# Performance work log

Measured on AMD Instinct MI355X. Metric: run time of the kernel, lower is better.

## Reference

```python
import jax, jax.numpy as jnp
import numpy as np

N, E, F_IN, HID, H, NCLS, L = 100000, 1600000, 128, 128, 4, 40, 2
C = HID // H  # per-head channels = 32
LN_EPS = 1e-5
SOFTMAX_EPS = 1e-16  # PyG softmax denominator epsilon


def setup_inputs() -> dict:
    key = jax.random.key(0)
    ks = jax.random.split(key, 8)
    s = 1.0 / np.sqrt(F_IN).astype(np.float32)
    return {
        "x": jax.random.normal(ks[0], (N, F_IN), jnp.float32),
        "edge_index": jax.random.randint(ks[1], (2, E), 0, N, jnp.int32),
        "Wq": jax.random.normal(ks[2], (L, F_IN, HID), jnp.float32) * s,
        "bq": jnp.zeros((L, HID), jnp.float32),
        "Wk": jax.random.normal(ks[3], (L, F_IN, HID), jnp.float32) * s,
        "bk": jnp.zeros((L, HID), jnp.float32),
        "Wv": jax.random.normal(ks[4], (L, F_IN, HID), jnp.float32) * s,
        "bv": jnp.zeros((L, HID), jnp.float32),
        "Ws": jax.random.normal(ks[5], (L, F_IN, HID), jnp.float32) * s,
        "bs": jnp.zeros((L, HID), jnp.float32),
        "gamma": jnp.ones((L, HID), jnp.float32),
        "beta": jnp.zeros((L, HID), jnp.float32),
        "Wout": jax.random.normal(ks[6], (HID, NCLS), jnp.float32) * (1.0 / np.sqrt(HID).astype(np.float32)),
        "bout": jnp.zeros((NCLS,), jnp.float32),
    }


def _transformer_conv(x, src, dst, Wq, bq, Wk, bk, Wv, bv, Ws, bs):
    # PyG TransformerConv, concat=False, root_weight=True, beta=False
    n = x.shape[0]
    q = (x @ Wq + bq).reshape(n, H, C)
    k = (x @ Wk + bk).reshape(n, H, C)
    v = (x @ Wv + bv).reshape(n, H, C)
    # per-edge attention logits: [E, H]
    alpha = jnp.einsum('ehc,ehc->eh', q[dst], k[src]) / np.sqrt(C).astype(np.float32)
    # segment softmax over incoming edges of each destination node
    amax = jax.ops.segment_max(alpha, dst, num_segments=n)        # [N, H]
    ex = jnp.exp(alpha - amax[dst])                               # [E, H]
    denom = jax.ops.segment_sum(ex, dst, num_segments=n)         # [N, H]
    w = ex / (denom[dst] + SOFTMAX_EPS)                           # [E, H]
    msg = v[src] * w[:, :, None]                                  # [E, H, C]
    out = jax.ops.segment_sum(msg, dst, num_segments=n)          # [N, H, C]
    out = out.mean(axis=1)                                        # concat=False -> head average, [N, C*?]. Here C*H==HID only via mean over H of C dims -> [N, C]
    # NOTE: concat=False averages heads -> [N, C]; skip proj maps in->C? In PyG, out_channels=hidden here,
    # so lin_* are Linear(in, heads*hidden)... but TransformerConv(in, hidden) means out_channels=hidden/?
    return out


def _conv(x, src, dst, Wq, bq, Wk, bk, Wv, bv, Ws, bs):
    # Faithful version with out_channels = HID per head? No: TransformerConv(in, hidden, heads, concat=False)
    # in PyG uses out_channels=hidden and lin_* : in -> heads*out_channels. To keep HID total width we model
    # per-head dim C = HID // H (standard multi-head factorization with same total width HID).
    n = x.shape[0]
    q = (x @ Wq + bq).reshape(n, H, C)
    k = (x @ Wk + bk).reshape(n, H, C)
    v = (x @ Wv + bv).reshape(n, H, C)
    alpha = jnp.einsum('ehc,ehc->eh', q[dst], k[src]) / np.sqrt(C).astype(np.float32)
    amax = jax.ops.segment_max(alpha, dst, num_segments=n)
    ex = jnp.exp(alpha - amax[dst])
    denom = jax.ops.segment_sum(ex, dst, num_segments=n)
    w = ex / (denom[dst] + SOFTMAX_EPS)
    msg = (v[src] * w[:, :, None]).reshape(-1, H * C)             # [E, HID]
    agg = jax.ops.segment_sum(msg, dst, num_segments=n)          # [N, HID]
    # concat=False -> mean over heads, then broadcast back is not what PyG does; PyG yields [N, out_channels].
    out = agg.reshape(n, H, C).mean(axis=1)                       # [N, C]
    out = jnp.tile(out, (1, H))                                   # widen back to HID? No — instead use skip of width HID.
    return out


def _conv_layer(x, src, dst, Wq, bq, Wk, bk, Wv, bv, Ws, bs):
    """TransformerConv(in, HID, heads=H, concat=False): lin_{q,k,v}: in -> H*HID is too wide for a
    memory target, so we use the equivalent standard factorization HID = H*C (per-head C), giving
    attention output [N, H, C]; concat=False head-mean is applied per head group and the result is
    projected residually via lin_skip (in -> HID)."""
    n = x.shape[0]
    q = (x @ Wq + bq).reshape(n, H, C)
    k = (x @ Wk + bk).reshape(n, H, C)
    v = (x @ Wv + bv).reshape(n, H, C)
    alpha = jnp.einsum('ehc,ehc->eh', q[dst], k[src]) / np.sqrt(C).astype(np.float32)
    amax = jax.ops.segment_max(alpha, dst, num_segments=n)        # [N, H]
    ex = jnp.exp(alpha - amax[dst])                               # [E, H]
    denom = jax.ops.segment_sum(ex, dst, num_segments=n)
    w = ex / (denom[dst] + SOFTMAX_EPS)
    msg = (v[src] * w[:, :, None]).reshape(-1, HID)               # [E, HID] (head-concat)
    agg = jax.ops.segment_sum(msg, dst, num_segments=n)          # [N, HID]
    return agg + x @ Ws + bs                                      # root/skip connection


def _layernorm(h, g, b):
    mu = h.mean(-1, keepdims=True)
    var = ((h - mu) ** 2).mean(-1, keepdims=True)
    return (h - mu) * jax.lax.rsqrt(var + LN_EPS) * g + b


def reference(x, edge_index, Wq, bq, Wk, bk, Wv, bv, Ws, bs, gamma, beta, Wout, bout):
    src, dst = edge_index[0], edge_index[1]
    h = x
    for l in range(L):  # fixed small layer count
        h = _conv_layer(h, src, dst, Wq[l], bq[l], Wk[l], bk[l], Wv[l], bv[l], Ws[l], bs[l])
        h = jax.nn.relu(_layernorm(h, gamma[l], beta[l]))
        # dropout is identity in eval mode
    return h @ Wout + bout  # [N, NCLS]
```

## Files before the change

kernel.cpp:

```cpp
#include <hip/hip_runtime.h>
#include <math.h>

#define N_NODES 100000
#define N_EDGES 1600000
#define NCLS_ 40
#define NSCAN_BLOCKS ((N_NODES + 1023) / 1024)
#define DRANGE 12500
#define SRCS_PAD (N_EDGES + 3 * N_NODES + 64)

#define QSCALE (0.17677669529663687f * 1.4426950408889634f)

#if __has_builtin(__builtin_amdgcn_exp2f)
#define EXP2(x) __builtin_amdgcn_exp2f(x)
#else
#define EXP2(x) exp2f(x)
#endif

typedef short bf16x8 __attribute__((ext_vector_type(8)));
typedef float f32x4 __attribute__((ext_vector_type(4)));

__device__ __forceinline__ unsigned short f2b(float f) {
    union { float f; unsigned u; } v; v.f = f;
    unsigned r = v.u + 0x7fffu + ((v.u >> 16) & 1u);
    return (unsigned short)(r >> 16);
}
__device__ __forceinline__ unsigned cvtpk(float x, float y) {
    unsigned r;
    asm("v_cvt_pk_bf16_f32 %0, %1, %2" : "=v"(r) : "v"(x), "v"(y));
    return r;
}
__device__ __forceinline__ float2 up2(unsigned u) {
    union { unsigned u; float f; } a, b;
    a.u = u << 16; b.u = u & 0xffff0000u;
    return make_float2(a.f, b.f);
}
__device__ __forceinline__ float b2f(unsigned short s) {
    union { unsigned u; float f; } v; v.u = ((unsigned)s) << 16;
    return v.f;
}


__global__ void zero_i32_kernel(int* __restrict__ p, int n) {
    int i = blockIdx.x * blockDim.x + threadIdx.x;
    if (i < n) p[i] = 0;
}

__global__ __launch_bounds__(256) void wconv_kernel(
    const float* __restrict__ Wq, const float* __restrict__ Wk,
    const float* __restrict__ Wv, const float* __restrict__ Ws,
    unsigned short* __restrict__ Wbf) {
    int tid = blockIdx.x * 256 + threadIdx.x;
    if (tid >= 131072) return;
    int k   = tid & 127;
    int n   = (tid >> 7) & 63;
    int g   = (tid >> 13) & 1;
    int mat = (tid >> 14) & 3;
    int l   = tid >> 16;
    const float* W = (mat == 0) ? Wq : (mat == 1) ? Wk : (mat == 2) ? Wv : Ws;
    float w = W[l * 16384 + k * 128 + g * 64 + n];
    if (mat == 0) w *= QSCALE;
    Wbf[tid] = f2b(w);
}

__global__ __launch_bounds__(256) void hist_kernel(
    const int* __restrict__ dst, int* __restrict__ deg) {
    int group = blockIdx.x & 7;
    int gblk  = blockIdx.x >> 3;
    int nblk  = gridDim.x >> 3;
    int lo = group * DRANGE, hi = lo + DRANGE;
    for (int i = gblk * 256 + threadIdx.x; i < N_EDGES; i += nblk * 256) {
        int d = dst[i];
        if (d >= lo && d < hi) atomicAdd(&deg[d], 1);
    }
}

__global__ __launch_bounds__(1024) void scan_block_kernel(
    const int* __restrict__ deg, int* __restrict__ rowptr, int* __restrict__ sums) {
    __shared__ int tmp[1024];
    int t = threadIdx.x;
    int i = blockIdx.x * 1024 + t;
    int v = (i < N_NODES) ? ((deg[i] + 3) & ~3) : 0;
    tmp[t] = v;
    __syncthreads();
    for (int d = 1; d < 1024; d <<= 1) {
        int add = (t >= d) ? tmp[t - d] : 0;
        __syncthreads();
        tmp[t] += add;
        __syncthreads();
    }
    if (i < N_NODES) rowptr[i] = tmp[t] - v;
    if (t == 1023) sums[blockIdx.x] = tmp[1023];
}

__global__ __launch_bounds__(128) void scan_sums_kernel(int* __restrict__ sums) {
    __shared__ int tmp[128];
    int t = threadIdx.x;
    int v = (t < NSCAN_BLOCKS) ? sums[t] : 0;
    tmp[t] = v;
    __syncthreads();
    for (int d = 1; d < 128; d <<= 1) {
        int add = (t >= d) ? tmp[t - d] : 0;
        __syncthreads();
        tmp[t] += add;
        __syncthreads();
    }
    if (t < NSCAN_BLOCKS) sums[t] = tmp[t] - v;
}

__global__ void scan_add_kernel(int* __restrict__ rowptr, const int* __restrict__ sums,
                                int* __restrict__ cursor) {
    int i = blockIdx.x * blockDim.x + threadIdx.x;
    if (i < N_NODES) {
        int val = rowptr[i] + sums[i >> 10];
        rowptr[i] = val;
        cursor[i] = val;
    }
}

__global__ __launch_bounds__(256) void scatter_kernel(
    const int* __restrict__ src, const int* __restrict__ dst,
    int* __restrict__ cursor, int* __restrict__ srcs) {
    int group = blockIdx.x & 7;
    int gblk  = blockIdx.x >> 3;
    int nblk  = gridDim.x >> 3;
    int lo = group * DRANGE, hi = lo + DRANGE;
    for (int i = gblk * 256 + threadIdx.x; i < N_EDGES; i += nblk * 256) {
        int d = dst[i];
        if (d >= lo && d < hi) {
            int pos = atomicAdd(&cursor[d], 1);
            srcs[pos] = src[i] << 10;
        }
    }
}

__global__ __launch_bounds__(512, 4) void gemm_qkvs_kernel(
    const void* __restrict__ Ap, int a_is_bf16,
    const unsigned short* __restrict__ Wbf,
    const float* __restrict__ b0, const float* __restrict__ b1,
    const float* __restrict__ b2, const float* __restrict__ b3,
    unsigned short* __restrict__ out) {
    __shared__ unsigned short Bs[2][64][138];
    int t = threadIdx.x;
    int row0 = blockIdx.x * 128;
    int wr = t >> 6, lane = t & 63;
    int ln = lane & 15, quad = lane >> 4;
    int node = row0 + wr * 16 + ln;
    int nodeC = (node < N_NODES) ? node : (N_NODES - 1);

    bf16x8 aF[4];
    if (a_is_bf16) {
        const unsigned short* ar = (const unsigned short*)Ap + (size_t)nodeC * 128;
        #pragma unroll
        for (int ks = 0; ks < 4; ++ks)
            aF[ks] = *(const bf16x8*)&ar[ks * 32 + quad * 8];
    } else {
        const float* ar = (const float*)Ap + (size_t)nodeC * 128;
        #pragma unroll
        for (int ks = 0; ks < 4; ++ks) {
            float4 f0 = *(const float4*)&ar[ks * 32 + quad * 8];
            float4 f1 = *(const float4*)&ar[ks * 32 + quad * 8 + 4];
            union { unsigned u[4]; bf16x8 v; } cv;
            cv.u[0] = cvtpk(f0.x, f0.y);
            cv.u[1] = cvtpk(f0.z, f0.w);
            cv.u[2] = cvtpk(f1.x, f1.y);
            cv.u[3] = cvtpk(f1.z, f1.w);
            aF[ks] = cv.v;
        }
    }

    ushort4 pf[4];
    {
        const unsigned short* Wg = Wbf;
        #pragma unroll
        for (int i = 0; i < 4; ++i) {
            int idx = t + i * 512;
            pf[i] = *(const ushort4*)&Wg[((idx >> 5) << 7) + ((idx & 31) << 2)];
        }
        #pragma unroll
        for (int i = 0; i < 4; ++i) {
            int idx = t + i * 512;
            *(ushort4*)&Bs[0][idx >> 5][(idx & 31) << 2] = pf[i];
        }
    }
    __syncthreads();

    bool ok = node < N_NODES;
    #pragma unroll
    for (int g = 0; g < 8; ++g) {
        int mat = g >> 1;
        int cur = g & 1;
        const float* bias = (mat == 0) ? b0 : (mat == 1) ? b1 : (mat == 2) ? b2 : b3;
        int cb = (g & 1) * 64;

        if (g < 7) {
            const unsigned short* Wg = Wbf + (size_t)(g + 1) * 8192;
            #pragma unroll
            for (int i = 0; i < 4; ++i) {
                int idx = t + i * 512;
                pf[i] = *(const ushort4*)&Wg[((idx >> 5) << 7) + ((idx & 31) << 2)];
            }
        }

        f32x4 acc[4];
        #pragma unroll
        for (int c = 0; c < 4; ++c) acc[c] = (f32x4){0.f, 0.f, 0.f, 0.f};
        #pragma unroll
        for (int ks = 0; ks < 4; ++ks) {
            int k0 = ks * 32 + quad * 8;
            #pragma unroll
            for (int c = 0; c < 4; ++c) {
                bf16x8 w = *(bf16x8*)&Bs[cur][c * 16 + ln][k0];
                acc[c] = __builtin_amdgcn_mfma_f32_16x16x32_bf16(w, aF[ks], acc[c], 0, 0, 0);
            }
        }

        #pragma unroll
        for (int c = 0; c < 4; ++c) {
            int ch = cb + c * 16 + quad * 4;
            float4 bb = *(const float4*)&bias[ch];
            float s = (mat == 0) ? QSCALE : 1.0f;
            float v0 = acc[c][0] + bb.x * s;
            float v1 = acc[c][1] + bb.y * s;
            float v2 = acc[c][2] + bb.z * s;
            float v3 = acc[c][3] + bb.w * s;
            int pos;
            if (mat == 0)      pos = ch;
            else if (mat == 3) pos = 384 + ch;
            else               pos = 128 + (ch << 1) + ((mat == 2) ? 4 : 0);
            if (ok) {
                uint2 wd;
                wd.x = cvtpk(v0, v1);
                wd.y = cvtpk(v2, v3);
                *(uint2*)&out[(size_t)node * 512 + pos] = wd;
            }
        }

        if (g < 7) {
            int nxt = cur ^ 1;
            #pragma unroll
            for (int i = 0; i < 4; ++i) {
                int idx = t + i * 512;
                *(ushort4*)&Bs[nxt][idx >> 5][(idx & 31) << 2] = pf[i];
            }
        }
        __syncthreads();
    }
}

#define EDGE(KV, ECOND) {                                            \
        float2 k01 = up2(KV.x), k23 = up2(KV.y);                     \
        float p = q01.x*k01.x + q01.y*k01.y + q23.x*k23.x + q23.y*k23.y; \
        p += __shfl_xor(p, 1);                                       \
        p += __shfl_xor(p, 2);                                       \
        p += __shfl_xor(p, 4);                                       \
        float e = (ECOND);                                           \
        float2 v01 = up2(KV.z), v23 = up2(KV.w);                     \
        a0 = fmaf(e, v01.x, a0); a1 = fmaf(e, v01.y, a1);            \
        a2 = fmaf(e, v23.x, a2); a3 = fmaf(e, v23.y, a3);            \
        dsum += e; }

__global__ __launch_bounds__(256) void edge_fused_kernel(
    const unsigned short* __restrict__ qkvs,
    const int* __restrict__ srcs, const int* __restrict__ rowptr,
    const int* __restrict__ deg,
    const float* __restrict__ gamma, const float* __restrict__ beta,
    unsigned short* __restrict__ hout) {
    int n = (blockIdx.x * 256 + threadIdx.x) >> 6;
    int lane = threadIdx.x & 63;
    if (n >= N_NODES) return;
    int half = lane >> 5, hl = lane & 31;
    const unsigned short* qrow = qkvs + (size_t)n * 512;
    uint2 qu = *(const uint2*)&qrow[4 * hl];
    float2 q01 = up2(qu.x), q23 = up2(qu.y);
    uint2 su = *(const uint2*)&qrow[384 + 4 * hl];
    float2 sk01 = up2(su.x), sk23 = up2(su.y);
    int e0 = rowptr[n];
    int rem = deg[n];
    const char* kbase = (const char*)qkvs + 256 + 16 * hl;
    const int* sb = srcs + e0 + 4 * half;
    float a0 = 0.f, a1 = 0.f, a2 = 0.f, a3 = 0.f, dsum = 0.f;

    int4 oc;
    if (rem >= 8) oc = *(const int4*)sb;
    while (rem >= 8) {
        int4 on;
        if (rem >= 16) on = *(const int4*)(sb + 8);
        uint4 kv0 = *(const uint4*)(kbase + (unsigned)oc.x);
        uint4 kv1 = *(const uint4*)(kbase + (unsigned)oc.y);
        uint4 kv2 = *(const uint4*)(kbase + (unsigned)oc.z);
        uint4 kv3 = *(const uint4*)(kbase + (unsigned)oc.w);
        EDGE(kv0, EXP2(p));
        EDGE(kv1, EXP2(p));
        EDGE(kv2, EXP2(p));
        EDGE(kv3, EXP2(p));
        oc = on; sb += 8; rem -= 8;
    }
    if (rem > 0) {
        int4 ot = *(const int4*)sb;
        int tb = 4 * half;
        uint4 kv0 = *(const uint4*)(kbase + (unsigned)ot.x);
        uint4 kv1 = *(const uint4*)(kbase + (unsigned)ot.y);
        uint4 kv2 = *(const uint4*)(kbase + (unsigned)ot.z);
        uint4 kv3 = *(const uint4*)(kbase + (unsigned)ot.w);
        EDGE(kv0, (tb + 0 < rem) ? EXP2(p) : 0.f);
        EDGE(kv1, (tb + 1 < rem) ? EXP2(p) : 0.f);
        EDGE(kv2, (tb + 2 < rem) ? EXP2(p) : 0.f);
        EDGE(kv3, (tb + 3 < rem) ? EXP2(p) : 0.f);
    }

    a0 += __shfl_xor(a0, 32); a1 += __shfl_xor(a1, 32);
    a2 += __shfl_xor(a2, 32); a3 += __shfl_xor(a3, 32);
    dsum += __shfl_xor(dsum, 32);
    float dinv = 1.0f / (dsum + 1e-16f);
    float o0 = a0 * dinv + sk01.x, o1 = a1 * dinv + sk01.y;
    float o2 = a2 * dinv + sk23.x, o3 = a3 * dinv + sk23.y;
    float sum = o0 + o1 + o2 + o3;
    for (int m = 1; m < 64; m <<= 1) sum += __shfl_xor(sum, m);
    float mu = sum * (1.0f / 256.0f);
    float d0 = o0 - mu, d1 = o1 - mu, d2 = o2 - mu, d3 = o3 - mu;
    float sq = d0 * d0 + d1 * d1 + d2 * d2 + d3 * d3;
    for (int m = 1; m < 64; m <<= 1) sq += __shfl_xor(sq, m);
    float rs = rsqrtf(sq * (1.0f / 256.0f) + 1e-5f);
    if (half == 0) {
        float4 g4 = *(const float4*)&gamma[4 * hl];
        float4 b4 = *(const float4*)&beta[4 * hl];
        float r0 = fmaxf(d0 * rs * g4.x + b4.x, 0.f);
        float r1 = fmaxf(d1 * rs * g4.y + b4.y, 0.f);
        float r2 = fmaxf(d2 * rs * g4.z + b4.z, 0.f);
        float r3 = fmaxf(d3 * rs * g4.w + b4.w, 0.f);
        uint2 w;
        w.x = cvtpk(r0, r1);
        w.y = cvtpk(r2, r3);
        *(uint2*)&hout[(size_t)n * 128 + 4 * hl] = w;
    }
}

__global__ __launch_bounds__(256) void out_gemm_kernel(
    const unsigned short* __restrict__ h, const float* __restrict__ Wout,
    const float* __restrict__ bout, float* __restrict__ out) {
    int wv = __builtin_amdgcn_readfirstlane((int)(threadIdx.x >> 6));
    int l = threadIdx.x & 63;
    int n = blockIdx.x * 64 + l;
    int jb = wv * 10;
    int nc = (n < N_NODES) ? n : (N_NODES - 1);
    const unsigned short* hrow = h + (size_t)nc * 128;
    uint4 hp[16];
    #pragma unroll
    for (int i = 0; i < 16; ++i) hp[i] = *(const uint4*)&hrow[i * 8];
    float acc[10];
    #pragma unroll
    for (int j = 0; j < 10; ++j) acc[j] = bout[jb + j];
    #pragma unroll
    for (int i = 0; i < 16; ++i) {
        float2 c01 = up2(hp[i].x), c23 = up2(hp[i].y);
        float2 c45 = up2(hp[i].z), c67 = up2(hp[i].w);
        float hc0 = c01.x, hc1 = c01.y, hc2 = c23.x, hc3 = c23.y;
        float hc4 = c45.x, hc5 = c45.y, hc6 = c67.x, hc7 = c67.y;
        #pragma unroll
        for (int j = 0; j < 10; ++j) {
            const float* wk = Wout + (i * 8) * NCLS_ + jb + j;
            acc[j] = fmaf(hc0, wk[0 * NCLS_], acc[j]);
            acc[j] = fmaf(hc1, wk[1 * NCLS_], acc[j]);
            acc[j] = fmaf(hc2, wk[2 * NCLS_], acc[j]);
            acc[j] = fmaf(hc3, wk[3 * NCLS_], acc[j]);
            acc[j] = fmaf(hc4, wk[4 * NCLS_], acc[j]);
            acc[j] = fmaf(hc5, wk[5 * NCLS_], acc[j]);
            acc[j] = fmaf(hc6, wk[6 * NCLS_], acc[j]);
            acc[j] = fmaf(hc7, wk[7 * NCLS_], acc[j]);
        }
    }
    if (n < N_NODES) {
        #pragma unroll
        for (int j = 0; j < 10; ++j) out[(size_t)n * NCLS_ + jb + j] = acc[j];
    }
}

extern "C" void kernel_launch(void* const* d_in, const int* in_sizes, int n_in,
                              void* d_out, int out_size, void* d_ws, size_t ws_size,
                              hipStream_t stream) {
    const float* x    = (const float*)d_in[0];
    const int*   ei   = (const int*)d_in[1];
    const int*   src  = ei;
    const int*   dst  = ei + N_EDGES;
    const float* Wq   = (const float*)d_in[2];
    const float* bq   = (const float*)d_in[3];
    const float* Wk   = (const float*)d_in[4];
    const float* bk   = (const float*)d_in[5];
    const float* Wv   = (const float*)d_in[6];
    const float* bv   = (const float*)d_in[7];
    const float* Wsk  = (const float*)d_in[8];
    const float* bsk  = (const float*)d_in[9];
    const float* gmm  = (const float*)d_in[10];
    const float* bta  = (const float*)d_in[11];
    const float* Wout = (const float*)d_in[12];
    const float* bout = (const float*)d_in[13];
    float* outp = (float*)d_out;

    char* p = (char*)d_ws;
    auto carve = [&](size_t bytes) {
        char* r = p;
        p += (bytes + 255) & ~(size_t)255;
        return r;
    };
    unsigned short* qkvs = (unsigned short*)carve((size_t)N_NODES * 512 * 2);
    unsigned short* h    = (unsigned short*)carve((size_t)N_NODES * 128 * 2);
    unsigned short* Wbf  = (unsigned short*)carve((size_t)131072 * 2);
    int* deg     = (int*)carve((size_t)N_NODES * 4);
    int* rowptr  = (int*)carve((size_t)(N_NODES + 1) * 4);
    int* cursor  = (int*)carve((size_t)N_NODES * 4);
    int* srcs    = (int*)carve((size_t)SRCS_PAD * 4);
    int* sums    = (int*)carve((size_t)NSCAN_BLOCKS * 4);

    wconv_kernel<<<512, 256, 0, stream>>>(Wq, Wk, Wv, Wsk, Wbf);

    zero_i32_kernel<<<(N_NODES + 255) / 256, 256, 0, stream>>>(deg, N_NODES);
    zero_i32_kernel<<<(SRCS_PAD + 255) / 256, 256, 0, stream>>>(srcs, SRCS_PAD);
    hist_kernel<<<2048, 256, 0, stream>>>(dst, deg);
    scan_block_kernel<<<NSCAN_BLOCKS, 1024, 0, stream>>>(deg, rowptr, sums);
    scan_sums_kernel<<<1, 128, 0, stream>>>(sums);
    scan_add_kernel<<<(N_NODES + 255) / 256, 256, 0, stream>>>(rowptr, sums, cursor);
    scatter_kernel<<<2048, 256, 0, stream>>>(src, dst, cursor, srcs);

    for (int l = 0; l < 2; ++l) {
        const void* hin = l ? (const void*)h : (const void*)x;
        gemm_qkvs_kernel<<<(N_NODES + 127) / 128, 512, 0, stream>>>(
            hin, l, Wbf + (size_t)l * 65536,
            bq + l * 128, bk + l * 128, bv + l * 128, bsk + l * 128, qkvs);
        edge_fused_kernel<<<(N_NODES + 3) / 4, 256, 0, stream>>>(
            qkvs, srcs, rowptr, deg, gmm + l * 128, bta + l * 128, h);
    }
    out_gemm_kernel<<<(N_NODES + 63) / 64, 256, 0, stream>>>(h, Wout, bout, outp);
}
```

Before: 681.5 us.

## Pre-swizzle weights into MFMA fragment order and fold srcs padding zeroing into scan

The weight conversion kernel now writes bf16 weights already in per-lane MFMA fragment order. The GEMM can then copy each weight tile to LDS with contiguous 16-byte loads and read fragments without a padded, strided layout. The output columns are permuted so each lane writes wider contiguous stores. The separate full zeroing of the padded srcs array is removed, and scan_add now zeroes only each node's padding slots plus a tail. This relies on the deg/rowptr padding convention matching the rest of the code.

New measurement: 671.8 us. Within noise of the previous version (-1.4%).

```diff
diff --git a/kernel.cpp b/kernel.cpp
--- a/kernel.cpp
+++ b/kernel.cpp
@@ -51,13 +51,18 @@
     unsigned short* __restrict__ Wbf) {
     int tid = blockIdx.x * 256 + threadIdx.x;
     if (tid >= 131072) return;
-    int k   = tid & 127;
-    int n   = (tid >> 7) & 63;
-    int g   = (tid >> 13) & 1;
-    int mat = (tid >> 14) & 3;
-    int l   = tid >> 16;
+    int j     = tid & 7;
+    int lane  = (tid >> 3) & 63;
+    int ks    = (tid >> 9) & 3;
+    int c     = (tid >> 11) & 3;
+    int ghalf = (tid >> 13) & 1;
+    int mat   = (tid >> 14) & 3;
+    int l     = tid >> 16;
+    int ln = lane & 15, quad = lane >> 4;
+    int col = ghalf * 64 + ((ln >> 2) << 4) + (c << 2) + (ln & 3);
+    int krow = (ks << 5) + (quad << 3) + j;
     const float* W = (mat == 0) ? Wq : (mat == 1) ? Wk : (mat == 2) ? Wv : Ws;
-    float w = W[l * 16384 + k * 128 + g * 64 + n];
+    float w = W[l * 16384 + krow * 128 + col];
     if (mat == 0) w *= QSCALE;
     Wbf[tid] = f2b(w);
 }
@@ -108,12 +113,20 @@
 }
 
 __global__ void scan_add_kernel(int* __restrict__ rowptr, const int* __restrict__ sums,
-                                int* __restrict__ cursor) {
+                                const int* __restrict__ deg,
+                                int* __restrict__ cursor, int* __restrict__ srcs) {
     int i = blockIdx.x * blockDim.x + threadIdx.x;
     if (i < N_NODES) {
         int val = rowptr[i] + sums[i >> 10];
         rowptr[i] = val;
         cursor[i] = val;
+        int d = deg[i];
+        int pad = ((d + 3) & ~3);
+        for (int j = d; j < pad; ++j) srcs[val + j] = 0;
+        if (i == N_NODES - 1) {
+            int end = val + pad;
+            for (int j = 0; j < 16; ++j) srcs[end + j] = 0;
+        }
     }
 }
 
@@ -139,7 +152,7 @@
     const float* __restrict__ b0, const float* __restrict__ b1,
     const float* __restrict__ b2, const float* __restrict__ b3,
     unsigned short* __restrict__ out) {
-    __shared__ unsigned short Bs[2][64][138];
+    __shared__ unsigned short WL[2][8192];
     int t = threadIdx.x;
     int row0 = blockIdx.x * 128;
     int wr = t >> 6, lane = t & 63;
@@ -168,19 +181,11 @@
         }
     }
 
-    ushort4 pf[4];
     {
-        const unsigned short* Wg = Wbf;
-        #pragma unroll
-        for (int i = 0; i < 4; ++i) {
-            int idx = t + i * 512;
-            pf[i] = *(const ushort4*)&Wg[((idx >> 5) << 7) + ((idx & 31) << 2)];
-        }
-        #pragma unroll
-        for (int i = 0; i < 4; ++i) {
-            int idx = t + i * 512;
-            *(ushort4*)&Bs[0][idx >> 5][(idx & 31) << 2] = pf[i];
-        }
+        const uint4* Wg4 = (const uint4*)Wbf;
+        uint4 a = Wg4[t * 2], b = Wg4[t * 2 + 1];
+        uint4* d4 = (uint4*)WL[0] + t * 2;
+        d4[0] = a; d4[1] = b;
     }
     __syncthreads();
 
@@ -192,13 +197,10 @@
         const float* bias = (mat == 0) ? b0 : (mat == 1) ? b1 : (mat == 2) ? b2 : b3;
         int cb = (g & 1) * 64;
 
+        uint4 pfa, pfb;
         if (g < 7) {
-            const unsigned short* Wg = Wbf + (size_t)(g + 1) * 8192;
-            #pragma unroll
-            for (int i = 0; i < 4; ++i) {
-                int idx = t + i * 512;
-                pf[i] = *(const ushort4*)&Wg[((idx >> 5) << 7) + ((idx & 31) << 2)];
-            }
+            const uint4* Wg4 = (const uint4*)(Wbf + (size_t)(g + 1) * 8192);
+            pfa = Wg4[t * 2]; pfb = Wg4[t * 2 + 1];
         }
 
         f32x4 acc[4];
@@ -206,42 +208,48 @@
         for (int c = 0; c < 4; ++c) acc[c] = (f32x4){0.f, 0.f, 0.f, 0.f};
         #pragma unroll
         for (int ks = 0; ks < 4; ++ks) {
-            int k0 = ks * 32 + quad * 8;
             #pragma unroll
             for (int c = 0; c < 4; ++c) {
-                bf16x8 w = *(bf16x8*)&Bs[cur][c * 16 + ln][k0];
+                bf16x8 w = *(bf16x8*)&WL[cur][((c * 4 + ks) * 64 + lane) * 8];
                 acc[c] = __builtin_amdgcn_mfma_f32_16x16x32_bf16(w, aF[ks], acc[c], 0, 0, 0);
             }
         }
 
-        #pragma unroll
-        for (int c = 0; c < 4; ++c) {
-            int ch = cb + c * 16 + quad * 4;
-            float4 bb = *(const float4*)&bias[ch];
+        if (ok) {
             float s = (mat == 0) ? QSCALE : 1.0f;
-            float v0 = acc[c][0] + bb.x * s;
-            float v1 = acc[c][1] + bb.y * s;
-            float v2 = acc[c][2] + bb.z * s;
-            float v3 = acc[c][3] + bb.w * s;
-            int pos;
-            if (mat == 0)      pos = ch;
-            else if (mat == 3) pos = 384 + ch;
-            else               pos = 128 + (ch << 1) + ((mat == 2) ? 4 : 0);
-            if (ok) {
-                uint2 wd;
-                wd.x = cvtpk(v0, v1);
-                wd.y = cvtpk(v2, v3);
-                *(uint2*)&out[(size_t)node * 512 + pos] = wd;
+            float v[16];
+            #pragma unroll
+            for (int c = 0; c < 4; ++c) {
+                float4 bb = *(const float4*)&bias[cb + quad * 16 + c * 4];
+                v[c * 4 + 0] = acc[c][0] + bb.x * s;
+                v[c * 4 + 1] = acc[c][1] + bb.y * s;
+                v[c * 4 + 2] = acc[c][2] + bb.z * s;
+                v[c * 4 + 3] = acc[c][3] + bb.w * s;
             }
+            unsigned pk[8];
+            #pragma unroll
+            for (int m = 0; m < 8; ++m) pk[m] = cvtpk(v[2 * m], v[2 * m + 1]);
+            unsigned short* orow = out + (size_t)node * 512;
+            if (mat == 0 || mat == 3) {
+                int base = (mat == 0 ? 0 : 384) + cb + quad * 16;
+                uint4 w0 = make_uint4(pk[0], pk[1], pk[2], pk[3]);
+                uint4 w1 = make_uint4(pk[4], pk[5], pk[6], pk[7]);
+                *(uint4*)&orow[base] = w0;
+                *(uint4*)&orow[base + 8] = w1;
+            } else {
+                int boff = (mat == 2) ? 4 : 0;
+                #pragma unroll
+                for (int c = 0; c < 4; ++c) {
+                    int pos = 128 + 8 * ((cb >> 2) + quad * 4 + c) + boff;
+                    uint2 wd; wd.x = pk[2 * c]; wd.y = pk[2 * c + 1];
+                    *(uint2*)&orow[pos] = wd;
+                }
+            }
         }
 
         if (g < 7) {
-            int nxt = cur ^ 1;
-            #pragma unroll
-            for (int i = 0; i < 4; ++i) {
-                int idx = t + i * 512;
-                *(ushort4*)&Bs[nxt][idx >> 5][(idx & 31) << 2] = pf[i];
-            }
+            uint4* d4 = (uint4*)WL[cur ^ 1] + t * 2;
+            d4[0] = pfa; d4[1] = pfb;
         }
         __syncthreads();
     }
@@ -414,11 +422,10 @@
     wconv_kernel<<<512, 256, 0, stream>>>(Wq, Wk, Wv, Wsk, Wbf);
 
     zero_i32_kernel<<<(N_NODES + 255) / 256, 256, 0, stream>>>(deg, N_NODES);
-    zero_i32_kernel<<<(SRCS_PAD + 255) / 256, 256, 0, stream>>>(srcs, SRCS_PAD);
     hist_kernel<<<2048, 256, 0, stream>>>(dst, deg);
     scan_block_kernel<<<NSCAN_BLOCKS, 1024, 0, stream>>>(deg, rowptr, sums);
     scan_sums_kernel<<<1, 128, 0, stream>>>(sums);
-    scan_add_kernel<<<(N_NODES + 255) / 256, 256, 0, stream>>>(rowptr, sums, cursor);
+    scan_add_kernel<<<(N_NODES + 255) / 256, 256, 0, stream>>>(rowptr, sums, deg, cursor, srcs);
     scatter_kernel<<<2048, 256, 0, stream>>>(src, dst, cursor, srcs);
 
     for (int l = 0; l < 2; ++l) {
```
